# Kernel optimization log

Hardware: AMD Instinct MI355X
Metric: run time of the kernel (lower is better)

## Reference

```python
import jax, jax.numpy as jnp
import numpy as np

UNITS = 1024
FORECAST = 128
FEATS = 128
BATCH = 256
WARMUP = 256


def setup_inputs() -> dict:
    key = jax.random.key(0)
    ks = jax.random.split(key, 4)
    s = 0.02  # small init scale to keep gates out of saturation
    return {
        "inputs": jax.random.normal(ks[0], (BATCH, WARMUP, FEATS), jnp.float32),
        "W_i": jax.random.normal(ks[1], (FEATS, 4 * UNITS), jnp.float32) * s,
        "W_h": jax.random.normal(ks[2], (UNITS, 4 * UNITS), jnp.float32) * s,
        "b": jnp.zeros((4 * UNITS,), jnp.float32),
        "W_d": jax.random.normal(ks[3], (UNITS, FEATS), jnp.float32) * s,
        "b_d": jnp.zeros((FEATS,), jnp.float32),
    }


def _lstm_cell(x, h, c, W_i, W_h, b):
    # Keras LSTMCell: gates ordered [input, forget, cell-candidate, output]
    z = x @ W_i + h @ W_h + b  # [B, 4U]
    i, f, g, o = jnp.split(z, 4, axis=-1)
    c_new = jax.nn.sigmoid(f) * c + jax.nn.sigmoid(i) * jnp.tanh(g)
    h_new = jax.nn.sigmoid(o) * jnp.tanh(c_new)
    return h_new, c_new


def reference(inputs, W_i, W_h, b, W_d, b_d):
    B = inputs.shape[0]
    U = W_h.shape[0]
    h0 = jnp.zeros((B, U), inputs.dtype)
    c0 = jnp.zeros((B, U), inputs.dtype)

    # warmup: run LSTM over the input sequence, keep final state
    def warm_step(carry, x_t):
        h, c = carry
        h, c = _lstm_cell(x_t, h, c, W_i, W_h, b)
        return (h, c), None

    (h, c), _ = jax.lax.scan(warm_step, (h0, c0), jnp.swapaxes(inputs, 0, 1))
    pred = h @ W_d + b_d  # first prediction [B, F]

    def fc_step(carry, _):
        h, c, p = carry
        h, c = _lstm_cell(p, h, c, W_i, W_h, b)
        p = h @ W_d + b_d
        return (h, c, p), p

    _, preds_rest = jax.lax.scan(fc_step, (h, c, pred), None, length=FORECAST - 1)
    preds = jnp.concatenate([pred[None], preds_rest], axis=0)  # [T, B, F]
    return jnp.swapaxes(preds, 0, 1)  # [B, T, F]
```

## Files before the change

kernel.cpp:

```cpp
#include <hip/hip_runtime.h>
#include <hip/hip_bf16.h>

#define UNITS 1024
#define FEATS 128
#define NG    4096
#define NSTEP 383
#define HS    262144
#define HSB   524288UL

#define OX   0UL
#define OWH  16777216UL
#define OWI  25165824UL
#define OWF  26214400UL
#define OWD  34603008UL
#define OBR  34865152UL
#define OBF  34881536UL
#define OH0  34897920UL
#define OHP  35422208UL
#define OHC  36470784UL
#define OCNT 68452352UL

typedef __attribute__((ext_vector_type(8))) short bf16x8;
typedef __attribute__((ext_vector_type(4))) float f32x4;
typedef __attribute__((ext_vector_type(4))) int i32x4;
typedef __attribute__((address_space(3))) char lds_char;
typedef __attribute__((address_space(1))) const char glb_char;

__device__ __forceinline__ void gload_lds16(const void* g, void* l) {
    __builtin_amdgcn_global_load_lds((glb_char*)g, (lds_char*)l, 16, 0, 0);
}
__device__ __forceinline__ int llc_load(const int* p) {
    int v;
    asm volatile("global_load_dword %0, %1, off sc0 sc1\n\ts_waitcnt vmcnt(0)"
                 : "=v"(v) : "v"(p) : "memory");
    return v;
}
__device__ __forceinline__ void l2_atomic_inc(int* p) {
    int one = 1;
    asm volatile("global_atomic_add %0, %1, off" :: "v"(p), "v"(one) : "memory");
}
__device__ __forceinline__ int l2_atomic_poll(int* p) {
    int v; int zero = 0;
    asm volatile("global_atomic_add %0, %1, %2, off sc0\n\ts_waitcnt vmcnt(0)"
                 : "=v"(v) : "v"(p), "v"(zero) : "memory");
    return v;
}

#define CFENCE asm volatile("" ::: "memory")
#define VMCNT0 asm volatile("s_waitcnt vmcnt(0)" ::: "memory")
#define L1INV  asm volatile("buffer_inv" ::: "memory")

__device__ __forceinline__ float sigf(float x) { return 1.0f / (1.0f + __expf(-x)); }
__device__ __forceinline__ float tanh_fast(float x) { return 2.0f / (1.0f + __expf(-2.0f * x)) - 1.0f; }

__device__ __forceinline__ int PK(int k) {
    return (k & ~15) | ((k & 3) << 2) | ((k >> 2) & 3);
}

__device__ __forceinline__ __hip_bfloat16* hist_ptr(char* ws, int s) {
    size_t off;
    if (s == 0)        off = OH0;
    else if (s <= 32)  off = OX  + (size_t)(s - 1) * HSB;
    else if (s <= 48)  off = OWH + (size_t)(s - 33) * HSB;
    else if (s <= 50)  off = OWI + (size_t)(s - 49) * HSB;
    else if (s <= 111) off = OHC + (size_t)(s - 51) * HSB;
    else               off = OWF + (size_t)(s - 112) * HSB;
    return (__hip_bfloat16*)(ws + off);
}

__device__ __forceinline__ void l2_sync(int* c, int target) {
    CFENCE;
    __syncthreads();
    if (threadIdx.x == 0) {
        l2_atomic_inc(c);
        while (l2_atomic_poll(c) < target) __builtin_amdgcn_s_sleep(1);
    }
    __syncthreads();
    CFENCE;
}

__device__ __forceinline__ void llc_sync(int* c, int target) {
    CFENCE;
    __syncthreads();
    if (threadIdx.x == 0) {
        atomicAdd(c, 1);
        while (llc_load(c) < target) __builtin_amdgcn_s_sleep(8);
    }
    __syncthreads();
    CFENCE;
}


__global__ void cvt_bf16(const float* __restrict__ in, __hip_bfloat16* __restrict__ out, int n) {
    int i = (blockIdx.x * blockDim.x + threadIdx.x) * 4;
    if (i >= n) return;
    float4 v = *(const float4*)(in + i);
    union { ushort4 u4; __hip_bfloat16 h[4]; } pk;
    pk.h[0] = __float2bfloat16(v.x);
    pk.h[1] = __float2bfloat16(v.y);
    pk.h[2] = __float2bfloat16(v.z);
    pk.h[3] = __float2bfloat16(v.w);
    *(ushort4*)(out + i) = pk.u4;
}

__global__ void build_whwi(const float* __restrict__ Wh, const float* __restrict__ Wi,
                           __hip_bfloat16* __restrict__ WhR, __hip_bfloat16* __restrict__ WiR) {
    int idx = blockIdx.x * 256 + threadIdx.x;
    int k = idx >> 12, col = idx & 4095;
    int j = ((col & 1023) << 2) | (col >> 10);
    if (k < 1024) WhR[(size_t)j * 1024 + k] = __float2bfloat16(Wh[(size_t)PK(k) * 4096 + col]);
    else          WiR[(size_t)j * 128 + (k - 1024)] = __float2bfloat16(Wi[(size_t)(k - 1024) * 4096 + col]);
}

__global__ void build_wd(const float* __restrict__ Wd, __hip_bfloat16* __restrict__ WdT) {
    int idx = blockIdx.x * 256 + threadIdx.x;
    int f = idx >> 10, k = idx & 1023;
    WdT[(size_t)f * 1024 + k] = __float2bfloat16(Wd[(size_t)PK(k) * 128 + f]);
}

__global__ void build_bias(const float* __restrict__ b, const float* __restrict__ bd,
                           const float* __restrict__ Wi, float* __restrict__ br, float* __restrict__ bf) {
    int j = blockIdx.x * 256 + threadIdx.x;
    int col = ((j & 3) << 10) | (j >> 2);
    float base = b[col];
    br[j] = base;
    float v = base;
    for (int q = 0; q < 128; ++q) v += bd[q] * Wi[(size_t)q * 4096 + col];
    bf[j] = v;
}

__global__ __launch_bounds__(256) void build_wf(const __hip_bfloat16* __restrict__ WhR,
                                                const __hip_bfloat16* __restrict__ WiR,
                                                const float* __restrict__ Wd,
                                                __hip_bfloat16* __restrict__ WfR) {
    const int j0 = blockIdx.x * 64, k0 = blockIdx.y * 64;
    const int tid = threadIdx.x, wave = tid >> 6, lane = tid & 63;
    const int wj = (wave >> 1) * 32, wk = (wave & 1) * 32;
    const int lr = lane & 15, lq = lane >> 4;
    const int TL = ((lr & 3) << 2) | (lr >> 2);
    f32x4 acc[2][2] = {};
    #pragma unroll
    for (int kc = 0; kc < 4; ++kc) {
        bf16x8 dfr[2], ifr[2];
        #pragma unroll
        for (int q2 = 0; q2 < 2; ++q2) {
            const float* p = Wd + (size_t)(k0 + wk + q2 * 16 + TL) * 128 + kc * 32 + lq * 8;
            __hip_bfloat16* dp = (__hip_bfloat16*)&dfr[q2];
            #pragma unroll
            for (int e = 0; e < 8; ++e) dp[e] = __float2bfloat16(p[e]);
            ifr[q2] = *(const bf16x8*)(WiR + (size_t)(j0 + wj + q2 * 16 + lr) * 128 + kc * 32 + lq * 8);
        }
        acc[0][0] = __builtin_amdgcn_mfma_f32_16x16x32_bf16(dfr[0], ifr[0], acc[0][0], 0, 0, 0);
        acc[0][1] = __builtin_amdgcn_mfma_f32_16x16x32_bf16(dfr[0], ifr[1], acc[0][1], 0, 0, 0);
        acc[1][0] = __builtin_amdgcn_mfma_f32_16x16x32_bf16(dfr[1], ifr[0], acc[1][0], 0, 0, 0);
        acc[1][1] = __builtin_amdgcn_mfma_f32_16x16x32_bf16(dfr[1], ifr[1], acc[1][1], 0, 0, 0);
    }
    #pragma unroll
    for (int cf = 0; cf < 2; ++cf)
        #pragma unroll
        for (int rf = 0; rf < 2; ++rf) {
            const int k = k0 + wk + cf * 16 + lq * 4;
            const int j = j0 + wj + rf * 16 + lr;
            const __hip_bfloat16* whp = WhR + (size_t)j * 1024 + k;
            __hip_bfloat16* wfp = WfR + (size_t)j * 1024 + k;
            #pragma unroll
            for (int e = 0; e < 4; ++e)
                wfp[e] = __float2bfloat16(acc[cf][rf][e] + __bfloat162float(whp[e]));
        }
}

__global__ __launch_bounds__(512, 2) void persist(char* ws) {
    const __hip_bfloat16* xb  = (const __hip_bfloat16*)(ws + OX);
    const __hip_bfloat16* whg = (const __hip_bfloat16*)(ws + OWH);
    const __hip_bfloat16* wig = (const __hip_bfloat16*)(ws + OWI);
    const __hip_bfloat16* wfg = (const __hip_bfloat16*)(ws + OWF);
    const float* brg = (const float*)(ws + OBR);
    const float* bfg = (const float*)(ws + OBF);
    __hip_bfloat16* hp0 = (__hip_bfloat16*)(ws + OHP);
    __hip_bfloat16* hp1 = hp0 + HS;

    __shared__ __hip_bfloat16 Als[9][32][128];
    __shared__ float Xl[4][2][4][2][256];
    __shared__ __hip_bfloat16 hTile[32][32];
    __shared__ int claimv[2];

    const int tid = threadIdx.x;

    if (tid == 0) {
        unsigned xcd;
        asm volatile("s_getreg_b32 %0, hwreg(HW_REG_XCC_ID, 0, 32)" : "=s"(xcd));
        int* slotc = (int*)(ws + OCNT + 1024);
        int slot = atomicAdd(slotc + (xcd & 7), 1);
        claimv[0] = (int)(xcd & 7);
        claimv[1] = slot & 31;
    }
    __syncthreads();
    const int grp  = claimv[0];
    const int tile = claimv[1];
    const int n0 = tile * 128;
    const int b0 = grp * 32;
    const int ublk = tile * 32;
    int* gcnt = (int*)(ws + OCNT) + grp * 32;
    int* glc  = (int*)(ws + OCNT + 1152);

    const int wave = tid >> 6, lane = tid & 63;
    const int cq = wave & 1, kh = wave >> 1;
    const int lr = lane & 15, lq = lane >> 4;

    bf16x8 w[4][9];
    #pragma unroll
    for (int tc = 0; tc < 4; ++tc) {
        const size_t row = (size_t)(n0 + cq * 64 + tc * 16 + lr);
        w[tc][0] = *(const bf16x8*)(wig + row * 128 + kh * 32 + lq * 8);
        #pragma unroll
        for (int c = 0; c < 8; ++c)
            w[tc][1 + c] = *(const bf16x8*)(whg + row * 1024 + c * 128 + kh * 32 + lq * 8);
    }
    float4 biasq = *(const float4*)(brg + n0 + cq * 64 + kh * 16 + lq * 4);

    float creg[2] = {0.f, 0.f};

    const int row_s = tid >> 4;
    const int gsw = (((tid & 15) ^ (row_s & 15)) << 3);
    char* sbase = (char*)&Als[0][0][0] + wave * 1024;

    gload_lds16(xb + (size_t)(b0 + row_s) * 32768 + gsw, sbase);

    for (int t = 0; t < NSTEP; ++t) {
        const bool fc = (t >= 256);
        const __hip_bfloat16* hsrc = fc ? hist_ptr(ws, t - 256) : ((t & 1) ? hp1 : hp0);
        __hip_bfloat16* hdst = (t >= 255) ? hist_ptr(ws, t - 255) : ((t & 1) ? hp0 : hp1);

        if (t == 256) {
            #pragma unroll
            for (int tc = 0; tc < 4; ++tc) {
                const size_t row = (size_t)(n0 + cq * 64 + tc * 16 + lr);
                #pragma unroll
                for (int c = 0; c < 8; ++c)
                    w[tc][1 + c] = *(const bf16x8*)(wfg + row * 1024 + c * 128 + kh * 32 + lq * 8);
            }
            biasq = *(const float4*)(bfg + n0 + cq * 64 + kh * 16 + lq * 4);
            VMCNT0;
            llc_sync(glc, 256);
        }

        L1INV;
        {
            const __hip_bfloat16* hsl = hsrc + (size_t)(b0 + row_s) * 1024 + gsw;
            #pragma unroll
            for (int c = 0; c < 8; ++c)
                gload_lds16(hsl + c * 128, sbase + (1 + c) * 8192);
        }

        f32x4 acc[4][2] = {};
        const int sc = ((kh * 4 + lq) ^ lr);
        {
            auto mf = [&](int r) {
                const bf16x8 a0 = *(const bf16x8*)&Als[r][lr][sc * 8];
                const bf16x8 a1 = *(const bf16x8*)&Als[r][lr + 16][sc * 8];
                #pragma unroll
                for (int tc = 0; tc < 4; ++tc) {
                    acc[tc][0] = __builtin_amdgcn_mfma_f32_16x16x32_bf16(w[tc][r], a0, acc[tc][0], 0, 0, 0);
                    acc[tc][1] = __builtin_amdgcn_mfma_f32_16x16x32_bf16(w[tc][r], a1, acc[tc][1], 0, 0, 0);
                }
            };
            asm volatile("s_waitcnt vmcnt(6)" ::: "memory");
            __builtin_amdgcn_s_barrier(); CFENCE;
            if (!fc) mf(0);
            mf(1); mf(2);
            asm volatile("s_waitcnt vmcnt(3)" ::: "memory");
            __builtin_amdgcn_s_barrier(); CFENCE;
            mf(3); mf(4); mf(5);
            asm volatile("s_waitcnt vmcnt(0)" ::: "memory");
            __builtin_amdgcn_s_barrier(); CFENCE;
            mf(6); mf(7); mf(8);
        }

        #pragma unroll
        for (int tc = 0; tc < 4; ++tc)
            #pragma unroll
            for (int rf = 0; rf < 2; ++rf)
                *(f32x4*)&Xl[kh][cq][tc][rf][lane * 4] = acc[tc][rf];
        __syncthreads();
        #pragma unroll
        for (int rf = 0; rf < 2; ++rf) {
            f32x4 z = {0.f, 0.f, 0.f, 0.f};
            #pragma unroll
            for (int k2 = 0; k2 < 4; ++k2)
                z += *(const f32x4*)&Xl[k2][cq][kh][rf][lane * 4];
            const float zi = z[0] + biasq.x;
            const float zf = z[1] + biasq.y;
            const float zg = z[2] + biasq.z;
            const float zo = z[3] + biasq.w;
            const float cn = sigf(zf) * creg[rf] + sigf(zi) * tanh_fast(zg);
            creg[rf] = cn;
            hTile[rf * 16 + lr][cq * 16 + lq * 4 + kh] = __float2bfloat16(sigf(zo) * tanh_fast(cn));
        }
        __syncthreads();

        if (tid < 128) {
            const int bl = tid >> 2, ch = tid & 3;
            *(i32x4*)(hdst + (size_t)(b0 + bl) * 1024 + ublk + ch * 8) =
                *(const i32x4*)&hTile[bl][ch * 8];
        }
        VMCNT0;

        if (t + 1 < 256)
            gload_lds16(xb + (size_t)(b0 + row_s) * 32768 + (size_t)(t + 1) * 128 + gsw, sbase);

        if (t + 1 < NSTEP)
            l2_sync(gcnt, 32 * (t + 1));
    }
}

__global__ __launch_bounds__(256) void pgemm(char* ws, float* __restrict__ out,
                                             const float* __restrict__ bd) {
    const int t = blockIdx.x >> 2;
    const int r0 = (blockIdx.x & 3) * 64;
    const int f0 = blockIdx.y * 64;
    const __hip_bfloat16* A = hist_ptr(ws, t);
    const __hip_bfloat16* Bw = (const __hip_bfloat16*)(ws + OWD);

    __shared__ __hip_bfloat16 Al[2][64 * 64];
    __shared__ __hip_bfloat16 Bl[2][64 * 64];

    const int tid = threadIdx.x;
    const int wave = tid >> 6, lane = tid & 63;
    const int whb = (wave >> 1) * 32, wcf = (wave & 1) * 32;
    const int lr = lane & 15, lq = lane >> 4;
    const int l8 = lane >> 3, cb = lane & 7;
    const int gsw = ((cb ^ l8) << 3);
    const int xk = lr & 7;

    f32x4 acc[2][2] = {};
    const int rA0 = whb + lr, rA1 = whb + lr + 16;
    const int rB0 = wcf + lr, rB1 = wcf + lr + 16;

    auto stage = [&](int buf, int k0) {
        #pragma unroll
        for (int l = 0; l < 2; ++l) {
            const int rt = wave * 16 + l * 8;
            const int row = rt + l8;
            gload_lds16(A + (size_t)(r0 + row) * 1024 + k0 + gsw, &Al[buf][rt * 64]);
            gload_lds16(Bw + (size_t)(f0 + row) * 1024 + k0 + gsw, &Bl[buf][rt * 64]);
        }
    };

    stage(0, 0);
    for (int kk = 0; kk < 16; ++kk) {
        const int buf = kk & 1;
        if (kk + 1 < 16) { stage(buf ^ 1, (kk + 1) << 6); asm volatile("s_waitcnt vmcnt(4)" ::: "memory"); }
        else             { VMCNT0; }
        CFENCE; __builtin_amdgcn_s_barrier(); CFENCE;
        #pragma unroll
        for (int ks = 0; ks < 2; ++ks) {
            const int g0 = ((ks * 4 + lq) ^ xk) << 3;
            bf16x8 a0 = *(const bf16x8*)&Al[buf][rA0 * 64 + g0];
            bf16x8 a1 = *(const bf16x8*)&Al[buf][rA1 * 64 + g0];
            bf16x8 w0 = *(const bf16x8*)&Bl[buf][rB0 * 64 + g0];
            bf16x8 w1 = *(const bf16x8*)&Bl[buf][rB1 * 64 + g0];
            acc[0][0] = __builtin_amdgcn_mfma_f32_16x16x32_bf16(w0, a0, acc[0][0], 0, 0, 0);
            acc[0][1] = __builtin_amdgcn_mfma_f32_16x16x32_bf16(w0, a1, acc[0][1], 0, 0, 0);
            acc[1][0] = __builtin_amdgcn_mfma_f32_16x16x32_bf16(w1, a0, acc[1][0], 0, 0, 0);
            acc[1][1] = __builtin_amdgcn_mfma_f32_16x16x32_bf16(w1, a1, acc[1][1], 0, 0, 0);
        }
        CFENCE; __builtin_amdgcn_s_barrier(); CFENCE;
    }
    #pragma unroll
    for (int cf = 0; cf < 2; ++cf) {
        const int fb = f0 + wcf + cf * 16 + lq * 4;
        const float4 b4 = *(const float4*)(bd + fb);
        #pragma unroll
        for (int rf = 0; rf < 2; ++rf) {
            const int b = r0 + whb + rf * 16 + lr;
            float4 o;
            o.x = acc[cf][rf][0] + b4.x;
            o.y = acc[cf][rf][1] + b4.y;
            o.z = acc[cf][rf][2] + b4.z;
            o.w = acc[cf][rf][3] + b4.w;
            *(float4*)(out + (size_t)b * 16384 + (size_t)t * 128 + fb) = o;
        }
    }
}


extern "C" void kernel_launch(void* const* d_in, const int* in_sizes, int n_in,
                              void* d_out, int out_size, void* d_ws, size_t ws_size,
                              hipStream_t stream) {
    const float* inputs = (const float*)d_in[0];
    const float* W_i    = (const float*)d_in[1];
    const float* W_h    = (const float*)d_in[2];
    const float* b      = (const float*)d_in[3];
    const float* W_d    = (const float*)d_in[4];
    const float* b_d    = (const float*)d_in[5];
    float* out = (float*)d_out;
    char* ws = (char*)d_ws;

    (void)hipMemsetAsync(ws + OHP, 0, HSB, stream);
    (void)hipMemsetAsync(ws + OCNT, 0, 2048, stream);

    cvt_bf16<<<8192, 256, 0, stream>>>(inputs, (__hip_bfloat16*)(ws + OX), 256 * 256 * 128);
    build_whwi<<<(1152 * 4096) / 256, 256, 0, stream>>>(
        W_h, W_i, (__hip_bfloat16*)(ws + OWH), (__hip_bfloat16*)(ws + OWI));
    build_wd<<<(128 * 1024) / 256, 256, 0, stream>>>(W_d, (__hip_bfloat16*)(ws + OWD));
    build_bias<<<16, 256, 0, stream>>>(b, b_d, W_i, (float*)(ws + OBR), (float*)(ws + OBF));
    build_wf<<<dim3(64, 16), 256, 0, stream>>>(
        (const __hip_bfloat16*)(ws + OWH), (const __hip_bfloat16*)(ws + OWI),
        W_d, (__hip_bfloat16*)(ws + OWF));

    char* wsp = ws;
    void* ka[] = { &wsp };
    (void)hipLaunchCooperativeKernel((void*)persist, dim3(256), dim3(512), ka, 0, stream);

    pgemm<<<dim3(512, 2), 256, 0, stream>>>(ws, out, b_d);
}
```

Measured before the change: 1.834 ms.

## Replace per-step group barrier with per-chunk dataflow flags

Drops the all-tiles atomic barrier at the end of each recurrent step. Each producer tile now increments a counter for its 128-unit chunk of h. Each wave polls only the counter for the chunk it needs, loads that chunk into LDS, and signals other waves through workgroup-scope LDS ready flags, so the MFMA accumulation can begin on chunks as they arrive. The aim is to cut the synchronization latency on the serial critical path. In exchange it adds spin loops on LDS flags, loses the previous vmcnt-staged overlap of loads, and depends on more subtle ordering for correctness of the double-buffered h history.

```diff
diff --git a/kernel.cpp b/kernel.cpp
--- a/kernel.cpp
+++ b/kernel.cpp
@@ -66,17 +66,6 @@
     else if (s <= 111) off = OHC + (size_t)(s - 51) * HSB;
     else               off = OWF + (size_t)(s - 112) * HSB;
     return (__hip_bfloat16*)(ws + off);
-}
-
-__device__ __forceinline__ void l2_sync(int* c, int target) {
-    CFENCE;
-    __syncthreads();
-    if (threadIdx.x == 0) {
-        l2_atomic_inc(c);
-        while (l2_atomic_poll(c) < target) __builtin_amdgcn_s_sleep(1);
-    }
-    __syncthreads();
-    CFENCE;
 }
 
 __device__ __forceinline__ void llc_sync(int* c, int target) {
@@ -183,13 +172,15 @@
     __shared__ float Xl[4][2][4][2][256];
     __shared__ __hip_bfloat16 hTile[32][32];
     __shared__ int claimv[2];
+    __shared__ int rdy[16];
 
     const int tid = threadIdx.x;
 
+    if (tid < 16) rdy[tid] = 0;
     if (tid == 0) {
         unsigned xcd;
         asm volatile("s_getreg_b32 %0, hwreg(HW_REG_XCC_ID, 0, 32)" : "=s"(xcd));
-        int* slotc = (int*)(ws + OCNT + 1024);
+        int* slotc = (int*)(ws + OCNT + 8192);
         int slot = atomicAdd(slotc + (xcd & 7), 1);
         claimv[0] = (int)(xcd & 7);
         claimv[1] = slot & 31;
@@ -200,8 +191,8 @@
     const int n0 = tile * 128;
     const int b0 = grp * 32;
     const int ublk = tile * 32;
-    int* gcnt = (int*)(ws + OCNT) + grp * 32;
-    int* glc  = (int*)(ws + OCNT + 1152);
+    int* fbase = (int*)(ws + OCNT + (size_t)grp * 1024);
+    int* glc   = (int*)(ws + OCNT + 8320);
 
     const int wave = tid >> 6, lane = tid & 63;
     const int cq = wave & 1, kh = wave >> 1;
@@ -220,11 +211,15 @@
 
     float creg[2] = {0.f, 0.f};
 
-    const int row_s = tid >> 4;
-    const int gsw = (((tid & 15) ^ (row_s & 15)) << 3);
-    char* sbase = (char*)&Als[0][0][0] + wave * 1024;
-
-    gload_lds16(xb + (size_t)(b0 + row_s) * 32768 + gsw, sbase);
+    if (wave == 0) {
+        #pragma unroll
+        for (int j = 0; j < 8; ++j) {
+            const int r32 = j * 4 + lq;
+            const int ce = ((lane & 15) ^ (r32 & 15)) << 3;
+            gload_lds16(xb + (size_t)(b0 + r32) * 32768 + ce,
+                        (char*)&Als[0][0][0] + j * 1024);
+        }
+    }
 
     for (int t = 0; t < NSTEP; ++t) {
         const bool fc = (t >= 256);
@@ -244,37 +239,42 @@
             llc_sync(glc, 256);
         }
 
+        if (t > 0 && lane == 0) {
+            int* fl = fbase + wave * 32;
+            while (l2_atomic_poll(fl) < 4 * t) __builtin_amdgcn_s_sleep(1);
+        }
         L1INV;
         {
-            const __hip_bfloat16* hsl = hsrc + (size_t)(b0 + row_s) * 1024 + gsw;
-            #pragma unroll
-            for (int c = 0; c < 8; ++c)
-                gload_lds16(hsl + c * 128, sbase + (1 + c) * 8192);
-        }
+            const __hip_bfloat16* srcb = hsrc + (size_t)b0 * 1024 + wave * 128;
+            char* dstc = (char*)&Als[1 + wave][0][0];
+            #pragma unroll
+            for (int j = 0; j < 8; ++j) {
+                const int r32 = j * 4 + lq;
+                const int ce = ((lane & 15) ^ (r32 & 15)) << 3;
+                gload_lds16(srcb + (size_t)r32 * 1024 + ce, dstc + j * 1024);
+            }
+        }
+        VMCNT0;
+        __hip_atomic_store(&rdy[wave], t + 1, __ATOMIC_RELEASE, __HIP_MEMORY_SCOPE_WORKGROUP);
 
         f32x4 acc[4][2] = {};
         const int sc = ((kh * 4 + lq) ^ lr);
-        {
-            auto mf = [&](int r) {
-                const bf16x8 a0 = *(const bf16x8*)&Als[r][lr][sc * 8];
-                const bf16x8 a1 = *(const bf16x8*)&Als[r][lr + 16][sc * 8];
-                #pragma unroll
-                for (int tc = 0; tc < 4; ++tc) {
-                    acc[tc][0] = __builtin_amdgcn_mfma_f32_16x16x32_bf16(w[tc][r], a0, acc[tc][0], 0, 0, 0);
-                    acc[tc][1] = __builtin_amdgcn_mfma_f32_16x16x32_bf16(w[tc][r], a1, acc[tc][1], 0, 0, 0);
-                }
-            };
-            asm volatile("s_waitcnt vmcnt(6)" ::: "memory");
-            __builtin_amdgcn_s_barrier(); CFENCE;
-            if (!fc) mf(0);
-            mf(1); mf(2);
-            asm volatile("s_waitcnt vmcnt(3)" ::: "memory");
-            __builtin_amdgcn_s_barrier(); CFENCE;
-            mf(3); mf(4); mf(5);
-            asm volatile("s_waitcnt vmcnt(0)" ::: "memory");
-            __builtin_amdgcn_s_barrier(); CFENCE;
-            mf(6); mf(7); mf(8);
-        }
+        auto wr_ = [&](int p) {
+            while (__hip_atomic_load(&rdy[p], __ATOMIC_ACQUIRE, __HIP_MEMORY_SCOPE_WORKGROUP) < t + 1) {}
+            __builtin_amdgcn_sched_barrier(0);
+        };
+        auto mfr = [&](int r) {
+            const bf16x8 a0 = *(const bf16x8*)&Als[r][lr][sc * 8];
+            const bf16x8 a1 = *(const bf16x8*)&Als[r][lr + 16][sc * 8];
+            #pragma unroll
+            for (int tc = 0; tc < 4; ++tc) {
+                acc[tc][0] = __builtin_amdgcn_mfma_f32_16x16x32_bf16(w[tc][r], a0, acc[tc][0], 0, 0, 0);
+                acc[tc][1] = __builtin_amdgcn_mfma_f32_16x16x32_bf16(w[tc][r], a1, acc[tc][1], 0, 0, 0);
+            }
+        };
+        if (!fc) { wr_(0); mfr(0); }
+        #pragma unroll
+        for (int r = 1; r <= 8; ++r) { wr_(r - 1); mfr(r); }
 
         #pragma unroll
         for (int tc = 0; tc < 4; ++tc)
@@ -304,12 +304,18 @@
                 *(const i32x4*)&hTile[bl][ch * 8];
         }
         VMCNT0;
-
-        if (t + 1 < 256)
-            gload_lds16(xb + (size_t)(b0 + row_s) * 32768 + (size_t)(t + 1) * 128 + gsw, sbase);
-
-        if (t + 1 < NSTEP)
-            l2_sync(gcnt, 32 * (t + 1));
+        __syncthreads();
+        if (tid == 0) l2_atomic_inc(fbase + (tile >> 2) * 32);
+
+        if (wave == 0 && t + 1 < 256) {
+            #pragma unroll
+            for (int j = 0; j < 8; ++j) {
+                const int r32 = j * 4 + lq;
+                const int ce = ((lane & 15) ^ (r32 & 15)) << 3;
+                gload_lds16(xb + (size_t)(b0 + r32) * 32768 + (size_t)(t + 1) * 128 + ce,
+                            (char*)&Als[0][0][0] + j * 1024);
+            }
+        }
     }
 }
 
@@ -397,7 +403,7 @@
     char* ws = (char*)d_ws;
 
     (void)hipMemsetAsync(ws + OHP, 0, HSB, stream);
-    (void)hipMemsetAsync(ws + OCNT, 0, 2048, stream);
+    (void)hipMemsetAsync(ws + OCNT, 0, 16384, stream);
 
     cvt_bf16<<<8192, 256, 0, stream>>>(inputs, (__hip_bfloat16*)(ws + OX), 256 * 256 * 128);
     build_whwi<<<(1152 * 4096) / 256, 256, 0, stream>>>(
```

New measurement: 1.758 ms. -4.2%, faster.
